# Kernel optimization log

Hardware: AMD Instinct MI355X
Metric: run time of the kernel (lower is better)

Reference implementation:

```python
import jax, jax.numpy as jnp
import numpy as np

N = 50000      # nodes
E = 800000     # edges (before self-loops)
H = 4          # heads
C = 64         # hidden_unit per head
IN = 256       # input_dim
OUT = 64       # output_dim
NEG = 0.2      # LeakyReLU slope in GATConv
EPS = 1e-5     # BatchNorm eps


def setup_inputs() -> dict:
    key = jax.random.key(0)
    ks = jax.random.split(key, 12)
    s = 0.05
    HC = H * C
    return {
        'x': jax.random.normal(ks[0], (N, IN), dtype=jnp.float32),
        'edge_index': jax.random.randint(ks[1], (2, E), 0, N, dtype=jnp.int64),
        # GATConv layer 1
        'W1': jax.random.normal(ks[2], (IN, HC), dtype=jnp.float32) * s,
        'att_src1': jax.random.normal(ks[3], (H, C), dtype=jnp.float32) * s,
        'att_dst1': jax.random.normal(ks[4], (H, C), dtype=jnp.float32) * s,
        'b1': jnp.zeros((HC,), jnp.float32),
        # GATConv layer 2
        'W2': jax.random.normal(ks[5], (HC, HC), dtype=jnp.float32) * s,
        'att_src2': jax.random.normal(ks[6], (H, C), dtype=jnp.float32) * s,
        'att_dst2': jax.random.normal(ks[7], (H, C), dtype=jnp.float32) * s,
        'b2': jnp.zeros((HC,), jnp.float32),
        # BatchNorms
        'g1': jnp.ones((HC,), jnp.float32), 'beta1': jnp.zeros((HC,), jnp.float32),
        'g2': jnp.ones((HC,), jnp.float32), 'beta2': jnp.zeros((HC,), jnp.float32),
        # final Linear
        'Wl': jax.random.normal(ks[8], (HC, OUT), dtype=jnp.float32) * s,
        'bl': jnp.zeros((OUT,), jnp.float32),
    }


def gat_layer(x, src, dst, W, a_src, a_dst, b):
    # x: [N, F_in] -> per-head features [N, H, C]
    xh = (x @ W).reshape(-1, H, C)
    alpha_src = jnp.einsum('nhc,hc->nh', xh, a_src)   # [N, H]
    alpha_dst = jnp.einsum('nhc,hc->nh', xh, a_dst)   # [N, H]
    e = jax.nn.leaky_relu(alpha_src[src] + alpha_dst[dst], NEG)  # [Etot, H]
    # segment softmax over edges grouped by destination node
    m = jax.ops.segment_max(e, dst, num_segments=N)              # [N, H]
    ex = jnp.exp(e - m[dst])
    den = jax.ops.segment_sum(ex, dst, num_segments=N)           # [N, H]
    alpha = ex / (den[dst] + 1e-16)                              # [Etot, H]
    # weighted scatter-add aggregation
    out = jax.ops.segment_sum(alpha[:, :, None] * xh[src], dst, num_segments=N)
    return out.reshape(-1, H * C) + b


def batchnorm(x, g, beta):
    mu = x.mean(axis=0)
    var = x.var(axis=0)
    return (x - mu) * jax.lax.rsqrt(var + EPS) * g + beta


def reference(x, edge_index, W1, att_src1, att_dst1, b1,
              W2, att_src2, att_dst2, b2, g1, beta1, g2, beta2, Wl, bl):
    # GATConv adds self-loops by default
    loops = jnp.arange(N, dtype=edge_index.dtype)
    src = jnp.concatenate([edge_index[0], loops])
    dst = jnp.concatenate([edge_index[1], loops])
    h = batchnorm(gat_layer(x, src, dst, W1, att_src1, att_dst1, b1), g1, beta1)
    # dropout is identity in eval mode
    h = batchnorm(gat_layer(h, src, dst, W2, att_src2, att_dst2, b2), g2, beta2)
    emb = h @ Wl + bl
    out = jax.nn.log_softmax(emb, axis=1)
    return (out, emb)
```

## Files before the change

kernel.cpp:

```cpp
#include <hip/hip_runtime.h>
#include <cstdint>

#define NNODES 50000
#define NEDGES 800000
#define ETOT   (NEDGES + NNODES)
#define HEADS 4
#define CH 64
#define HC 256
#define INDIM 256
#define OUTDIM 64
#define NEG_SLOPE 0.2f
#define BN_EPS 1e-5f
#define NB 128

typedef unsigned short u16;
typedef unsigned int u32;
typedef __attribute__((ext_vector_type(8))) short short8;
typedef __attribute__((ext_vector_type(8))) unsigned short ushort8v;
typedef __attribute__((ext_vector_type(4))) float floatx4;

__device__ inline float bf2f(u16 u) {
    union { unsigned int i; float f; } c;
    c.i = ((unsigned int)u) << 16;
    return c.f;
}
__device__ inline u16 f2bf(float f) {
    union { float f; unsigned int i; } c;
    c.f = f;
    unsigned int u = c.i + 0x7fff + ((c.i >> 16) & 1);
    return (u16)(u >> 16);
}
__device__ __host__ inline int pos256(int b) {
    int h = b >> 6, c = b & 63;
    return h * 64 + (c & 15) * 4 + (c >> 4);
}
__device__ inline void async16(u16* lds, const u16* g) {
    __builtin_amdgcn_global_load_lds(
        (const __attribute__((address_space(1))) unsigned int*)g,
        (__attribute__((address_space(3))) unsigned int*)lds,
        16, 0, 0);
}


__global__ void hist_kernel(const int* __restrict__ ei, int* __restrict__ cnt) {
    int t = blockIdx.x * blockDim.x + threadIdx.x;
    if (t >= ETOT) return;
    int d = (t < NEDGES) ? ei[NEDGES + t] : (t - NEDGES);
    atomicAdd(&cnt[d], 1);
}

__global__ void scan1_kernel(const int* __restrict__ cnt, int* __restrict__ row_off,
                             int* __restrict__ blockSums) {
    __shared__ int tsum[256];
    const int tid = threadIdx.x;
    const int base = blockIdx.x * 4096 + tid * 16;
    int local[16];
    int run = 0;
#pragma unroll
    for (int i = 0; i < 16; ++i) {
        int idx = base + i;
        int v = (idx < NNODES) ? cnt[idx] : 0;
        local[i] = run;
        run += v;
    }
    tsum[tid] = run;
    __syncthreads();
    for (int d = 1; d < 256; d <<= 1) {
        int v = (tid >= d) ? tsum[tid - d] : 0;
        __syncthreads();
        tsum[tid] += v;
        __syncthreads();
    }
    int excl = (tid == 0) ? 0 : tsum[tid - 1];
#pragma unroll
    for (int i = 0; i < 16; ++i) {
        int idx = base + i;
        if (idx < NNODES) row_off[idx] = excl + local[i];
    }
    if (tid == 0) blockSums[blockIdx.x] = tsum[255];
}

__global__ void scan2_kernel(int* __restrict__ row_off, const int* __restrict__ blockSums,
                             int* __restrict__ nxt) {
    __shared__ int sprefix;
    if (threadIdx.x == 0) {
        int p = 0;
        for (int b = 0; b < (int)blockIdx.x; ++b) p += blockSums[b];
        sprefix = p;
    }
    __syncthreads();
    int prefix = sprefix;
    int base = blockIdx.x * 4096 + threadIdx.x * 16;
#pragma unroll
    for (int i = 0; i < 16; ++i) {
        int idx = base + i;
        if (idx < NNODES) {
            int v = row_off[idx] + prefix;
            row_off[idx] = v;
            nxt[idx] = v;
        }
    }
    if (blockIdx.x == 0 && threadIdx.x == 0) row_off[NNODES] = ETOT;
}

#define FILL_S (ETOT / 4)
__global__ void fill_csr_kernel(const int* __restrict__ ei, int* __restrict__ nxt,
                                int* __restrict__ csr_src) {
    int t = blockIdx.x * blockDim.x + threadIdx.x;
    if (t >= FILL_S) return;
    int s[4], d[4], p[4];
#pragma unroll
    for (int k = 0; k < 4; ++k) {
        int e = t + k * FILL_S;
        if (e < NEDGES) { s[k] = ei[e]; d[k] = ei[NEDGES + e]; }
        else            { s[k] = d[k] = e - NEDGES; }
    }
#pragma unroll
    for (int k = 0; k < 4; ++k) p[k] = atomicAdd(&nxt[d[k]], 1);
#pragma unroll
    for (int k = 0; k < 4; ++k) csr_src[p[k]] = s[k];
}


__global__ void wcast_kernel(const float* __restrict__ W, u16* __restrict__ Wt,
                             int K, int Ncols) {
    int t = blockIdx.x * blockDim.x + threadIdx.x;
    if (t >= K * Ncols) return;
    int k = t / Ncols, n = t - k * Ncols;
    Wt[n * K + k] = f2bf(W[t]);
}


template <bool AF32>
__global__ __launch_bounds__(256)
void gemm_gat_kernel(const void* __restrict__ Ap, const u16* __restrict__ Bt,
                     const float* __restrict__ bias,
                     const float* __restrict__ att_s, const float* __restrict__ att_d,
                     u16* __restrict__ xhp, float* __restrict__ asrc,
                     float* __restrict__ adst, int M, int K) {
    __shared__ u16 As[128 * 32];
    __shared__ u16 Bs[128 * 32];
    const int tid = threadIdx.x;
    const int wave = tid >> 6, lane = tid & 63;
    const int q15 = lane & 15, quad = lane >> 4;
    const int rowBase = blockIdx.y * 128;
    const int colBase = blockIdx.x * 128;
    const int waveM = (wave >> 1) * 64, waveN = (wave & 1) * 64;
    const int head = blockIdx.x * 2 + (wave & 1);

    floatx4 acc[4][4];
    floatx4 zero = {0.f, 0.f, 0.f, 0.f};
#pragma unroll
    for (int i = 0; i < 4; ++i)
#pragma unroll
        for (int j = 0; j < 4; ++j) acc[i][j] = zero;

    for (int kt = 0; kt < K; kt += 32) {
        if constexpr (AF32) {
            const float* A32 = (const float*)Ap;
#pragma unroll
            for (int rnd = 0; rnd < 4; ++rnd) {
                int slot = rnd * 256 + tid;
                int r = slot >> 3, c4 = (slot & 7) * 4;
                int ar = rowBase + r; if (ar >= M) ar = M - 1;
                float4 fv = *(const float4*)&A32[(size_t)ar * K + kt + c4];
                ushort4 o;
                o.x = f2bf(fv.x); o.y = f2bf(fv.y); o.z = f2bf(fv.z); o.w = f2bf(fv.w);
                *(ushort4*)&As[r * 32 + c4] = o;
            }
#pragma unroll
            for (int q = 0; q < 2; ++q) {
                int e8 = (wave * 2 + q) * 64 + lane;
                int r = e8 >> 2, c = (e8 & 3) * 8;
                async16(&Bs[(wave * 2 + q) * 512], &Bt[(size_t)(colBase + r) * K + kt + c]);
            }
        } else {
            const u16* A16 = (const u16*)Ap;
#pragma unroll
            for (int q = 0; q < 2; ++q) {
                int e8 = (wave * 2 + q) * 64 + lane;
                int r = e8 >> 2, c = (e8 & 3) * 8;
                int ar = rowBase + r; if (ar >= M) ar = M - 1;
                async16(&As[(wave * 2 + q) * 512], &A16[(size_t)ar * K + kt + c]);
                async16(&Bs[(wave * 2 + q) * 512], &Bt[(size_t)(colBase + r) * K + kt + c]);
            }
        }
        __syncthreads();

        short8 af[4], bfr[4];
#pragma unroll
        for (int i = 0; i < 4; ++i)
            af[i] = *(const short8*)&As[(waveM + i * 16 + q15) * 32 + quad * 8];
#pragma unroll
        for (int j = 0; j < 4; ++j)
            bfr[j] = *(const short8*)&Bs[(waveN + j * 16 + q15) * 32 + quad * 8];
#pragma unroll
        for (int i = 0; i < 4; ++i)
#pragma unroll
            for (int j = 0; j < 4; ++j)
                acc[i][j] = __builtin_amdgcn_mfma_f32_16x16x32_bf16(af[i], bfr[j], acc[i][j], 0, 0, 0);
        __syncthreads();
    }

    float bv[4], atsv[4], atdv[4];
#pragma unroll
    for (int j = 0; j < 4; ++j) {
        int gcol = colBase + waveN + j * 16 + q15;
        bv[j] = bias ? bias[gcol] : 0.f;
        int hc = head * CH + j * 16 + q15;
        atsv[j] = att_s[hc];
        atdv[j] = att_d[hc];
    }
    const int pbase = head * 64 + q15 * 4;

#pragma unroll
    for (int i = 0; i < 4; ++i) {
#pragma unroll
        for (int rr = 0; rr < 4; ++rr) {
            int grow = rowBase + waveM + i * 16 + quad * 4 + rr;
            float v[4];
#pragma unroll
            for (int j = 0; j < 4; ++j) v[j] = acc[i][j][rr] + bv[j];
            float s = v[0] * atsv[0] + v[1] * atsv[1] + v[2] * atsv[2] + v[3] * atsv[3];
            float d = v[0] * atdv[0] + v[1] * atdv[1] + v[2] * atdv[2] + v[3] * atdv[3];
#pragma unroll
            for (int off = 1; off <= 8; off <<= 1) {
                s += __shfl_xor(s, off, 64);
                d += __shfl_xor(d, off, 64);
            }
            ushort4 o;
            o.x = f2bf(v[0]); o.y = f2bf(v[1]); o.z = f2bf(v[2]); o.w = f2bf(v[3]);
            if (grow < M) {
                *(ushort4*)&xhp[(size_t)grow * HC + pbase] = o;
                if (q15 == 0) {
                    asrc[grow * 4 + head] = s;
                    adst[grow * 4 + head] = d;
                }
            }
        }
    }
}


__global__ __launch_bounds__(256)
void aggregate_kernel(const int* __restrict__ row_off, const int* __restrict__ csr_src,
                      const float* __restrict__ asrc, const float* __restrict__ adst,
                      const u16* __restrict__ xhp, const float* __restrict__ bias,
                      u16* __restrict__ out) {
    __shared__ int eb[4][512];
    const int g = threadIdx.x >> 6;
    const int lane = threadIdx.x & 63;
    const int d = blockIdx.x * 4 + g;
    const int eh = lane >> 5;
    const int L = lane & 31;
    const int h = L >> 3;
    const int g8 = L & 7;
    const u32 pb = (u32)(h * 128 + g8 * 16);
    int* my = &eb[g][0];

    const int start = row_off[d], end = row_off[d + 1];
    const float4 ad4 = *(const float4*)&adst[d * 4];
    float acc[8] = {0.f, 0.f, 0.f, 0.f, 0.f, 0.f, 0.f, 0.f};
    float den = 0.f;

#define ACC4(W, Q, J0) { u32 dw_ = (u32)(Q); \
        acc[J0]     += (W) * __int_as_float(dw_ << 16); \
        acc[(J0)+1] += (W) * __int_as_float(dw_ & 0xffff0000u); }

    for (int base = start; base < end; base += 64) {
        const int cnt = min(64, end - base);
        int4 pack = {0, 0, 0, 0};
        int svv = 0;
        if (lane < cnt) {
            svv = csr_src[base + lane];
            float4 as4 = *(const float4*)&asrc[svv * 4];
            float e0 = as4.x + ad4.x; e0 = e0 > 0.f ? e0 : NEG_SLOPE * e0;
            float e1 = as4.y + ad4.y; e1 = e1 > 0.f ? e1 : NEG_SLOPE * e1;
            float e2 = as4.z + ad4.z; e2 = e2 > 0.f ? e2 : NEG_SLOPE * e2;
            float e3 = as4.w + ad4.w; e3 = e3 > 0.f ? e3 : NEG_SLOPE * e3;
            pack.x = __float_as_int(__expf(e0));
            pack.y = __float_as_int(__expf(e1));
            pack.z = __float_as_int(__expf(e2));
            pack.w = __float_as_int(__expf(e3));
        }
        *(int4*)&my[lane * 8] = pack;
        my[lane * 8 + 4] = svv;
        asm volatile("s_waitcnt lgkmcnt(0)" ::: "memory");
        __builtin_amdgcn_sched_barrier(0);

        const int cntp = (cnt + 1) & ~1;
        int k = 0;
        for (; k + 7 < cntp; k += 8) {
            float wv[4]; int sa[4];
#pragma unroll
            for (int p = 0; p < 4; ++p) {
                int idx = (k + 2 * p + eh) * 8;
                wv[p] = __int_as_float(my[idx + h]);
                sa[p] = my[idx + 4];
            }
            int4 gv[4];
#pragma unroll
            for (int p = 0; p < 4; ++p) {
                u32 off = ((u32)sa[p] << 9) + pb;
                gv[p] = *(const int4*)((const char*)xhp + off);
            }
#pragma unroll
            for (int p = 0; p < 4; ++p) {
                float w = wv[p];
                den += w;
                ACC4(w, gv[p].x, 0); ACC4(w, gv[p].y, 2);
                ACC4(w, gv[p].z, 4); ACC4(w, gv[p].w, 6);
            }
        }
        for (; k < cntp; k += 2) {
            int idx = (k + eh) * 8;
            float w = __int_as_float(my[idx + h]);
            int s = my[idx + 4];
            u32 off = ((u32)s << 9) + pb;
            int4 gvv = *(const int4*)((const char*)xhp + off);
            den += w;
            ACC4(w, gvv.x, 0); ACC4(w, gvv.y, 2);
            ACC4(w, gvv.z, 4); ACC4(w, gvv.w, 6);
        }
    }
#undef ACC4

#pragma unroll
    for (int i = 0; i < 8; ++i) acc[i] += __shfl_xor(acc[i], 32, 64);
    den += __shfl_xor(den, 32, 64);

    if (eh == 0) {
        float inv = 1.f / (den + 1e-16f);
        const int cb = h * 64 + g8 * 2;
        ushort8v o;
#pragma unroll
        for (int j = 0; j < 8; ++j)
            o[j] = f2bf(acc[j] * inv + bias[cb + (j >> 2) + (j & 3) * 16]);
        *(ushort8v*)&out[(size_t)d * HC + h * 64 + g8 * 8] = o;
    }
}


__global__ __launch_bounds__(256)
void bn_stats_kernel(const u16* __restrict__ x, float* __restrict__ part) {
    const int tid = threadIdx.x;
    float s[8] = {}, s2[8] = {};
    const size_t total = (size_t)NNODES * HC;
    const size_t stride = (size_t)NB * 256 * 8;
    for (size_t f = ((size_t)blockIdx.x * 256 + tid) * 8; f < total; f += stride) {
        ushort8v v = *(const ushort8v*)&x[f];
#pragma unroll
        for (int i = 0; i < 8; ++i) {
            float t = bf2f(v[i]);
            s[i] += t;
            s2[i] += t * t;
        }
    }
#pragma unroll
    for (int i = 0; i < 8; ++i) {
        s[i] += __shfl_xor(s[i], 32, 64);
        s2[i] += __shfl_xor(s2[i], 32, 64);
    }
    __shared__ float red[4][512];
    const int wave = tid >> 6, lane = tid & 63;
    if (lane < 32) {
#pragma unroll
        for (int i = 0; i < 8; ++i) {
            red[wave][lane * 8 + i] = s[i];
            red[wave][256 + lane * 8 + i] = s2[i];
        }
    }
    __syncthreads();
    for (int j = tid; j < 512; j += 256)
        part[(size_t)blockIdx.x * 512 + j] = red[0][j] + red[1][j] + red[2][j] + red[3][j];
}


__global__ __launch_bounds__(256)
void fold_kernel(const float* __restrict__ W, const float* __restrict__ part,
                 const float* __restrict__ g, const float* __restrict__ beta,
                 const float* __restrict__ baseBias,
                 u16* __restrict__ Wt, float* __restrict__ biasOut, int Ncols) {
    __shared__ float sh[256];
    __shared__ float stat2[2];
    const int b = blockIdx.x;
    const int tid = threadIdx.x;
    if (b < 256) {
        const int p = pos256(b);
        const int wave = tid >> 6, lane = tid & 63;
        if (wave < 2) {
            int off = wave * 256;
            float v = part[(size_t)lane * 512 + off + p] + part[(size_t)(lane + 64) * 512 + off + p];
#pragma unroll
            for (int o = 1; o <= 32; o <<= 1) v += __shfl_xor(v, o, 64);
            if (lane == 0) stat2[wave] = v;
        }
        __syncthreads();
        float mu = stat2[0] * (1.f / NNODES);
        float var = stat2[1] * (1.f / NNODES) - mu * mu;
        float rg = rsqrtf(var + BN_EPS) * g[b];
        for (int n = tid; n < Ncols; n += 256)
            Wt[n * 256 + p] = f2bf(W[b * Ncols + n] * rg);
    } else {
        const int p = pos256(tid);
        float sum = 0.f, sq = 0.f;
        for (int k = 0; k < NB; ++k) {
            sum += part[(size_t)k * 512 + p];
            sq += part[(size_t)k * 512 + 256 + p];
        }
        float mu = sum * (1.f / NNODES);
        float var = sq * (1.f / NNODES) - mu * mu;
        float rg = rsqrtf(var + BN_EPS) * g[tid];
        sh[tid] = beta[tid] - mu * rg;
        __syncthreads();
        if (tid < Ncols) {
            float acc = baseBias ? baseBias[tid] : 0.f;
            for (int k = 0; k < 256; ++k) acc += sh[k] * W[k * Ncols + tid];
            biasOut[tid] = acc;
        }
    }
}


__global__ __launch_bounds__(256)
void final_ls_kernel(const u16* __restrict__ A, const u16* __restrict__ Bt,
                     const float* __restrict__ bias,
                     float* __restrict__ emb, float* __restrict__ out, int M) {
    __shared__ u16 As[128 * 32];
    __shared__ u16 Bs[64 * 32];
    const int tid = threadIdx.x;
    const int wave = tid >> 6, lane = tid & 63;
    const int q15 = lane & 15, quad = lane >> 4;
    const int rowBase = blockIdx.x * 128;

    floatx4 acc[2][4];
    floatx4 zero = {0.f, 0.f, 0.f, 0.f};
#pragma unroll
    for (int i = 0; i < 2; ++i)
#pragma unroll
        for (int j = 0; j < 4; ++j) acc[i][j] = zero;

    for (int kt = 0; kt < 256; kt += 32) {
#pragma unroll
        for (int rnd = 0; rnd < 2; ++rnd) {
            int slot = rnd * 256 + wave * 64 + lane;
            int r = slot >> 2;
            int c = (slot & 3) * 8;
            int ar = rowBase + r; if (ar >= M) ar = M - 1;
            async16(&As[(rnd * 256 + wave * 64) * 8], &A[(size_t)ar * 256 + kt + c]);
        }
        {
            int slot = wave * 64 + lane;
            int r = slot >> 2;
            int c = (slot & 3) * 8;
            async16(&Bs[(wave * 64) * 8], &Bt[(size_t)r * 256 + kt + c]);
        }
        __syncthreads();

        short8 af[2], bfr[4];
#pragma unroll
        for (int i = 0; i < 2; ++i)
            af[i] = *(const short8*)&As[(wave * 32 + i * 16 + q15) * 32 + quad * 8];
#pragma unroll
        for (int j = 0; j < 4; ++j)
            bfr[j] = *(const short8*)&Bs[(j * 16 + q15) * 32 + quad * 8];
#pragma unroll
        for (int i = 0; i < 2; ++i)
#pragma unroll
            for (int j = 0; j < 4; ++j)
                acc[i][j] = __builtin_amdgcn_mfma_f32_16x16x32_bf16(af[i], bfr[j], acc[i][j], 0, 0, 0);
        __syncthreads();
    }

#pragma unroll
    for (int i = 0; i < 2; ++i) {
#pragma unroll
        for (int rr = 0; rr < 4; ++rr) {
            float v[4];
#pragma unroll
            for (int j = 0; j < 4; ++j) v[j] = acc[i][j][rr] + bias[j * 16 + q15];
            float m = fmaxf(fmaxf(v[0], v[1]), fmaxf(v[2], v[3]));
#pragma unroll
            for (int off = 1; off <= 8; off <<= 1) m = fmaxf(m, __shfl_xor(m, off, 64));
            float s = __expf(v[0] - m) + __expf(v[1] - m) + __expf(v[2] - m) + __expf(v[3] - m);
#pragma unroll
            for (int off = 1; off <= 8; off <<= 1) s += __shfl_xor(s, off, 64);
            float ls = m + logf(s);
            int grow = rowBase + wave * 32 + i * 16 + quad * 4 + rr;
            if (grow < M) {
#pragma unroll
                for (int j = 0; j < 4; ++j) {
                    int col = j * 16 + q15;
                    emb[(size_t)grow * OUTDIM + col] = v[j];
                    out[(size_t)grow * OUTDIM + col] = v[j] - ls;
                }
            }
        }
    }
}


extern "C" void kernel_launch(void* const* d_in, const int* in_sizes, int n_in,
                              void* d_out, int out_size, void* d_ws, size_t ws_size,
                              hipStream_t stream) {
    const float* x   = (const float*)d_in[0];
    const int*   ei  = (const int*)d_in[1];
    const float* W1  = (const float*)d_in[2];
    const float* at_s1 = (const float*)d_in[3];
    const float* at_d1 = (const float*)d_in[4];
    const float* b1  = (const float*)d_in[5];
    const float* W2  = (const float*)d_in[6];
    const float* at_s2 = (const float*)d_in[7];
    const float* at_d2 = (const float*)d_in[8];
    const float* b2  = (const float*)d_in[9];
    const float* g1  = (const float*)d_in[10];
    const float* be1 = (const float*)d_in[11];
    const float* g2  = (const float*)d_in[12];
    const float* be2 = (const float*)d_in[13];
    const float* Wl  = (const float*)d_in[14];
    const float* bl  = (const float*)d_in[15];

    float* out = (float*)d_out;
    float* emb = out + (size_t)NNODES * OUTDIM;

    char* ws = (char*)d_ws;
    size_t off = 0;
    auto alloc = [&](size_t bytes) {
        void* p = ws + off;
        off += (bytes + 255) & ~(size_t)255;
        return p;
    };
    int*   cnt     = (int*)alloc((size_t)NNODES * 4);
    int*   row_off = (int*)alloc((size_t)(NNODES + 1) * 4);
    int*   nxt     = (int*)alloc((size_t)NNODES * 4);
    int*   bsums   = (int*)alloc(64 * 4);
    int*   csr_src = (int*)alloc((size_t)ETOT * 4);
    float* asrc    = (float*)alloc((size_t)NNODES * 4 * 4);
    float* adst    = (float*)alloc((size_t)NNODES * 4 * 4);
    u16*   xhp     = (u16*)alloc((size_t)NNODES * HC * 2);
    u16*   ag_bf   = (u16*)alloc((size_t)NNODES * HC * 2);
    u16*   w1t     = (u16*)alloc((size_t)HC * INDIM * 2);
    u16*   w2t     = (u16*)alloc((size_t)HC * HC * 2);
    u16*   wlt     = (u16*)alloc((size_t)OUTDIM * HC * 2);
    float* part    = (float*)alloc((size_t)NB * 512 * 4);
    float* bias2   = (float*)alloc(HC * 4);
    float* blp     = (float*)alloc(OUTDIM * 4);

    const int scanBlocks = (NNODES + 4095) / 4096;
    const int eBlocks = (ETOT + 255) / 256;

    hipMemsetAsync(cnt, 0, (size_t)NNODES * 4, stream);
    hist_kernel<<<eBlocks, 256, 0, stream>>>(ei, cnt);
    scan1_kernel<<<scanBlocks, 256, 0, stream>>>(cnt, row_off, bsums);
    scan2_kernel<<<scanBlocks, 256, 0, stream>>>(row_off, bsums, nxt);
    fill_csr_kernel<<<(FILL_S + 255) / 256, 256, 0, stream>>>(ei, nxt, csr_src);

    wcast_kernel<<<(INDIM * HC + 255) / 256, 256, 0, stream>>>(W1, w1t, INDIM, HC);

    dim3 gemmGrid(2, (NNODES + 127) / 128);

    gemm_gat_kernel<true><<<gemmGrid, 256, 0, stream>>>(x, w1t, nullptr, at_s1, at_d1,
                                                        xhp, asrc, adst, NNODES, INDIM);
    aggregate_kernel<<<NNODES / 4, 256, 0, stream>>>(row_off, csr_src, asrc, adst, xhp, b1, ag_bf);
    bn_stats_kernel<<<NB, 256, 0, stream>>>(ag_bf, part);
    fold_kernel<<<257, 256, 0, stream>>>(W2, part, g1, be1, nullptr, w2t, bias2, HC);

    gemm_gat_kernel<false><<<gemmGrid, 256, 0, stream>>>(ag_bf, w2t, bias2, at_s2, at_d2,
                                                         xhp, asrc, adst, NNODES, HC);
    aggregate_kernel<<<NNODES / 4, 256, 0, stream>>>(row_off, csr_src, asrc, adst, xhp, b2, ag_bf);
    bn_stats_kernel<<<NB, 256, 0, stream>>>(ag_bf, part);
    fold_kernel<<<257, 256, 0, stream>>>(Wl, part, g2, be2, bl, wlt, blp, OUTDIM);

    final_ls_kernel<<<(NNODES + 127) / 128, 256, 0, stream>>>(ag_bf, wlt, blp, emb, out, NNODES);
}
```

Baseline: 495.0 us.

## Merge CSR build and BN stats/fold stages into cooperative grid-synced kernels

Replaces the memset, histogram, two scan kernels, CSR fill and weight cast with one cooperative kernel that separates phases with grid.sync. It also merges each bn_stats and fold pair into one cooperative kernel. The aim is to cut kernel launch overhead and inter-kernel gaps across many small stages. In exchange, the CSR work runs on a fixed grid of 1024 blocks with grid-stride loops, and grid barriers add cost; the scan phases use only a few blocks while the rest wait at the barrier.

```diff
diff --git a/kernel.cpp b/kernel.cpp
--- a/kernel.cpp
+++ b/kernel.cpp
@@ -1,5 +1,8 @@
 #include <hip/hip_runtime.h>
+#include <hip/hip_cooperative_groups.h>
 #include <cstdint>
+
+namespace cg = cooperative_groups;
 
 #define NNODES 50000
 #define NEDGES 800000
@@ -12,6 +15,8 @@
 #define NEG_SLOPE 0.2f
 #define BN_EPS 1e-5f
 #define NB 128
+#define CSR_BLOCKS 1024
+#define CSR_GSZ (CSR_BLOCKS * 256)
 
 typedef unsigned short u16;
 typedef unsigned int u32;
@@ -40,94 +45,109 @@
         (__attribute__((address_space(3))) unsigned int*)lds,
         16, 0, 0);
 }
-
-
-__global__ void hist_kernel(const int* __restrict__ ei, int* __restrict__ cnt) {
-    int t = blockIdx.x * blockDim.x + threadIdx.x;
-    if (t >= ETOT) return;
-    int d = (t < NEDGES) ? ei[NEDGES + t] : (t - NEDGES);
-    atomicAdd(&cnt[d], 1);
-}
-
-__global__ void scan1_kernel(const int* __restrict__ cnt, int* __restrict__ row_off,
-                             int* __restrict__ blockSums) {
+__device__ inline int ld_devi(const int* p) {
+    return __hip_atomic_load(p, __ATOMIC_RELAXED, __HIP_MEMORY_SCOPE_AGENT);
+}
+__device__ inline float ld_devf(const float* p) {
+    return __hip_atomic_load(p, __ATOMIC_RELAXED, __HIP_MEMORY_SCOPE_AGENT);
+}
+
+
+#define FILL_S (ETOT / 4)
+
+__global__ __launch_bounds__(256)
+void csr_build_kernel(const int* __restrict__ ei, int* __restrict__ cnt,
+                      int* __restrict__ row_off, int* __restrict__ nxt,
+                      int* __restrict__ bsums, int* __restrict__ csr_src,
+                      const float* __restrict__ W1, u16* __restrict__ w1t) {
+    cg::grid_group grid = cg::this_grid();
+    const int tid = threadIdx.x;
+    const int gt = blockIdx.x * 256 + tid;
     __shared__ int tsum[256];
-    const int tid = threadIdx.x;
-    const int base = blockIdx.x * 4096 + tid * 16;
-    int local[16];
-    int run = 0;
-#pragma unroll
-    for (int i = 0; i < 16; ++i) {
-        int idx = base + i;
-        int v = (idx < NNODES) ? cnt[idx] : 0;
-        local[i] = run;
-        run += v;
-    }
-    tsum[tid] = run;
-    __syncthreads();
-    for (int d = 1; d < 256; d <<= 1) {
-        int v = (tid >= d) ? tsum[tid - d] : 0;
-        __syncthreads();
-        tsum[tid] += v;
-        __syncthreads();
-    }
-    int excl = (tid == 0) ? 0 : tsum[tid - 1];
-#pragma unroll
-    for (int i = 0; i < 16; ++i) {
-        int idx = base + i;
-        if (idx < NNODES) row_off[idx] = excl + local[i];
-    }
-    if (tid == 0) blockSums[blockIdx.x] = tsum[255];
-}
-
-__global__ void scan2_kernel(int* __restrict__ row_off, const int* __restrict__ blockSums,
-                             int* __restrict__ nxt) {
     __shared__ int sprefix;
-    if (threadIdx.x == 0) {
-        int p = 0;
-        for (int b = 0; b < (int)blockIdx.x; ++b) p += blockSums[b];
-        sprefix = p;
-    }
-    __syncthreads();
-    int prefix = sprefix;
-    int base = blockIdx.x * 4096 + threadIdx.x * 16;
-#pragma unroll
-    for (int i = 0; i < 16; ++i) {
-        int idx = base + i;
-        if (idx < NNODES) {
-            int v = row_off[idx] + prefix;
-            row_off[idx] = v;
-            nxt[idx] = v;
-        }
-    }
-    if (blockIdx.x == 0 && threadIdx.x == 0) row_off[NNODES] = ETOT;
-}
-
-#define FILL_S (ETOT / 4)
-__global__ void fill_csr_kernel(const int* __restrict__ ei, int* __restrict__ nxt,
-                                int* __restrict__ csr_src) {
-    int t = blockIdx.x * blockDim.x + threadIdx.x;
-    if (t >= FILL_S) return;
-    int s[4], d[4], p[4];
-#pragma unroll
-    for (int k = 0; k < 4; ++k) {
-        int e = t + k * FILL_S;
-        if (e < NEDGES) { s[k] = ei[e]; d[k] = ei[NEDGES + e]; }
-        else            { s[k] = d[k] = e - NEDGES; }
-    }
-#pragma unroll
-    for (int k = 0; k < 4; ++k) p[k] = atomicAdd(&nxt[d[k]], 1);
-#pragma unroll
-    for (int k = 0; k < 4; ++k) csr_src[p[k]] = s[k];
-}
-
-
-__global__ void wcast_kernel(const float* __restrict__ W, u16* __restrict__ Wt,
-                             int K, int Ncols) {
-    int t = blockIdx.x * blockDim.x + threadIdx.x;
-    if (t >= K * Ncols) return;
-    int k = t / Ncols, n = t - k * Ncols;
-    Wt[n * K + k] = f2bf(W[t]);
+
+    for (int i = gt; i < NNODES; i += CSR_GSZ) cnt[i] = 0;
+    for (int i = gt; i < INDIM * HC; i += CSR_GSZ) {
+        int k = i >> 8, n = i & 255;
+        w1t[n * INDIM + k] = f2bf(W1[i]);
+    }
+    __threadfence();
+    grid.sync();
+
+    for (int t = gt; t < ETOT; t += CSR_GSZ) {
+        int d = (t < NEDGES) ? ei[NEDGES + t] : (t - NEDGES);
+        atomicAdd(&cnt[d], 1);
+    }
+    __threadfence();
+    grid.sync();
+
+    const int scanBlocks = (NNODES + 4095) / 4096;
+    if ((int)blockIdx.x < scanBlocks) {
+        const int base = blockIdx.x * 4096 + tid * 16;
+        int local[16];
+        int run = 0;
+#pragma unroll
+        for (int i = 0; i < 16; ++i) {
+            int idx = base + i;
+            int v = (idx < NNODES) ? ld_devi(&cnt[idx]) : 0;
+            local[i] = run;
+            run += v;
+        }
+        tsum[tid] = run;
+        __syncthreads();
+        for (int dd = 1; dd < 256; dd <<= 1) {
+            int v = (tid >= dd) ? tsum[tid - dd] : 0;
+            __syncthreads();
+            tsum[tid] += v;
+            __syncthreads();
+        }
+        int excl = (tid == 0) ? 0 : tsum[tid - 1];
+#pragma unroll
+        for (int i = 0; i < 16; ++i) {
+            int idx = base + i;
+            if (idx < NNODES) row_off[idx] = excl + local[i];
+        }
+        if (tid == 0) bsums[blockIdx.x] = tsum[255];
+    }
+    __threadfence();
+    grid.sync();
+
+    if ((int)blockIdx.x < scanBlocks) {
+        if (tid == 0) {
+            int p = 0;
+            for (int b = 0; b < (int)blockIdx.x; ++b) p += ld_devi(&bsums[b]);
+            sprefix = p;
+        }
+        __syncthreads();
+        int prefix = sprefix;
+        int base = blockIdx.x * 4096 + tid * 16;
+#pragma unroll
+        for (int i = 0; i < 16; ++i) {
+            int idx = base + i;
+            if (idx < NNODES) {
+                int v = row_off[idx] + prefix;
+                row_off[idx] = v;
+                nxt[idx] = v;
+            }
+        }
+        if (blockIdx.x == 0 && tid == 0) row_off[NNODES] = ETOT;
+    }
+    __threadfence();
+    grid.sync();
+
+    if (gt < FILL_S) {
+        int s[4], d[4], p[4];
+#pragma unroll
+        for (int k = 0; k < 4; ++k) {
+            int e = gt + k * FILL_S;
+            if (e < NEDGES) { s[k] = ei[e]; d[k] = ei[NEDGES + e]; }
+            else            { s[k] = d[k] = e - NEDGES; }
+        }
+#pragma unroll
+        for (int k = 0; k < 4; ++k) p[k] = atomicAdd(&nxt[d[k]], 1);
+#pragma unroll
+        for (int k = 0; k < 4; ++k) csr_src[p[k]] = s[k];
+    }
 }
 
 
@@ -342,55 +362,57 @@
 
 
 __global__ __launch_bounds__(256)
-void bn_stats_kernel(const u16* __restrict__ x, float* __restrict__ part) {
+void statsfold_kernel(const u16* __restrict__ x, float* __restrict__ part,
+                      const float* __restrict__ W, const float* __restrict__ g,
+                      const float* __restrict__ beta, const float* __restrict__ baseBias,
+                      u16* __restrict__ Wt, float* __restrict__ biasOut, int Ncols) {
+    cg::grid_group grid = cg::this_grid();
     const int tid = threadIdx.x;
-    float s[8] = {}, s2[8] = {};
-    const size_t total = (size_t)NNODES * HC;
-    const size_t stride = (size_t)NB * 256 * 8;
-    for (size_t f = ((size_t)blockIdx.x * 256 + tid) * 8; f < total; f += stride) {
-        ushort8v v = *(const ushort8v*)&x[f];
-#pragma unroll
-        for (int i = 0; i < 8; ++i) {
-            float t = bf2f(v[i]);
-            s[i] += t;
-            s2[i] += t * t;
-        }
-    }
-#pragma unroll
-    for (int i = 0; i < 8; ++i) {
-        s[i] += __shfl_xor(s[i], 32, 64);
-        s2[i] += __shfl_xor(s2[i], 32, 64);
-    }
     __shared__ float red[4][512];
-    const int wave = tid >> 6, lane = tid & 63;
-    if (lane < 32) {
-#pragma unroll
-        for (int i = 0; i < 8; ++i) {
-            red[wave][lane * 8 + i] = s[i];
-            red[wave][256 + lane * 8 + i] = s2[i];
-        }
-    }
-    __syncthreads();
-    for (int j = tid; j < 512; j += 256)
-        part[(size_t)blockIdx.x * 512 + j] = red[0][j] + red[1][j] + red[2][j] + red[3][j];
-}
-
-
-__global__ __launch_bounds__(256)
-void fold_kernel(const float* __restrict__ W, const float* __restrict__ part,
-                 const float* __restrict__ g, const float* __restrict__ beta,
-                 const float* __restrict__ baseBias,
-                 u16* __restrict__ Wt, float* __restrict__ biasOut, int Ncols) {
     __shared__ float sh[256];
     __shared__ float stat2[2];
+
+    if (blockIdx.x < NB) {
+        float s[8] = {}, s2[8] = {};
+        const size_t total = (size_t)NNODES * HC;
+        const size_t stride = (size_t)NB * 256 * 8;
+        for (size_t f = ((size_t)blockIdx.x * 256 + tid) * 8; f < total; f += stride) {
+            ushort8v v = *(const ushort8v*)&x[f];
+#pragma unroll
+            for (int i = 0; i < 8; ++i) {
+                float t = bf2f(v[i]);
+                s[i] += t;
+                s2[i] += t * t;
+            }
+        }
+#pragma unroll
+        for (int i = 0; i < 8; ++i) {
+            s[i] += __shfl_xor(s[i], 32, 64);
+            s2[i] += __shfl_xor(s2[i], 32, 64);
+        }
+        const int wave = tid >> 6, lane = tid & 63;
+        if (lane < 32) {
+#pragma unroll
+            for (int i = 0; i < 8; ++i) {
+                red[wave][lane * 8 + i] = s[i];
+                red[wave][256 + lane * 8 + i] = s2[i];
+            }
+        }
+        __syncthreads();
+        for (int j = tid; j < 512; j += 256)
+            part[(size_t)blockIdx.x * 512 + j] = red[0][j] + red[1][j] + red[2][j] + red[3][j];
+    }
+    __threadfence();
+    grid.sync();
+
     const int b = blockIdx.x;
-    const int tid = threadIdx.x;
     if (b < 256) {
         const int p = pos256(b);
         const int wave = tid >> 6, lane = tid & 63;
         if (wave < 2) {
             int off = wave * 256;
-            float v = part[(size_t)lane * 512 + off + p] + part[(size_t)(lane + 64) * 512 + off + p];
+            float v = ld_devf(&part[(size_t)lane * 512 + off + p]) +
+                      ld_devf(&part[(size_t)(lane + 64) * 512 + off + p]);
 #pragma unroll
             for (int o = 1; o <= 32; o <<= 1) v += __shfl_xor(v, o, 64);
             if (lane == 0) stat2[wave] = v;
@@ -405,8 +427,8 @@
         const int p = pos256(tid);
         float sum = 0.f, sq = 0.f;
         for (int k = 0; k < NB; ++k) {
-            sum += part[(size_t)k * 512 + p];
-            sq += part[(size_t)k * 512 + 256 + p];
+            sum += ld_devf(&part[(size_t)k * 512 + p]);
+            sq += ld_devf(&part[(size_t)k * 512 + 256 + p]);
         }
         float mu = sum * (1.f / NNODES);
         float var = sq * (1.f / NNODES) - mu * mu;
@@ -546,30 +568,36 @@
     float* bias2   = (float*)alloc(HC * 4);
     float* blp     = (float*)alloc(OUTDIM * 4);
 
-    const int scanBlocks = (NNODES + 4095) / 4096;
-    const int eBlocks = (ETOT + 255) / 256;
-
-    hipMemsetAsync(cnt, 0, (size_t)NNODES * 4, stream);
-    hist_kernel<<<eBlocks, 256, 0, stream>>>(ei, cnt);
-    scan1_kernel<<<scanBlocks, 256, 0, stream>>>(cnt, row_off, bsums);
-    scan2_kernel<<<scanBlocks, 256, 0, stream>>>(row_off, bsums, nxt);
-    fill_csr_kernel<<<(FILL_S + 255) / 256, 256, 0, stream>>>(ei, nxt, csr_src);
-
-    wcast_kernel<<<(INDIM * HC + 255) / 256, 256, 0, stream>>>(W1, w1t, INDIM, HC);
+    {
+        void* a[] = {(void*)&ei, (void*)&cnt, (void*)&row_off, (void*)&nxt,
+                     (void*)&bsums, (void*)&csr_src, (void*)&W1, (void*)&w1t};
+        hipLaunchCooperativeKernel((void*)csr_build_kernel, dim3(CSR_BLOCKS), dim3(256),
+                                   a, 0, stream);
+    }
 
     dim3 gemmGrid(2, (NNODES + 127) / 128);
+    const float* nbias = nullptr;
+    int ncols1 = HC, ncols2 = OUTDIM;
 
     gemm_gat_kernel<true><<<gemmGrid, 256, 0, stream>>>(x, w1t, nullptr, at_s1, at_d1,
                                                         xhp, asrc, adst, NNODES, INDIM);
     aggregate_kernel<<<NNODES / 4, 256, 0, stream>>>(row_off, csr_src, asrc, adst, xhp, b1, ag_bf);
-    bn_stats_kernel<<<NB, 256, 0, stream>>>(ag_bf, part);
-    fold_kernel<<<257, 256, 0, stream>>>(W2, part, g1, be1, nullptr, w2t, bias2, HC);
+    {
+        void* a[] = {(void*)&ag_bf, (void*)&part, (void*)&W2, (void*)&g1, (void*)&be1,
+                     (void*)&nbias, (void*)&w2t, (void*)&bias2, (void*)&ncols1};
+        hipLaunchCooperativeKernel((void*)statsfold_kernel, dim3(257), dim3(256),
+                                   a, 0, stream);
+    }
 
     gemm_gat_kernel<false><<<gemmGrid, 256, 0, stream>>>(ag_bf, w2t, bias2, at_s2, at_d2,
                                                          xhp, asrc, adst, NNODES, HC);
     aggregate_kernel<<<NNODES / 4, 256, 0, stream>>>(row_off, csr_src, asrc, adst, xhp, b2, ag_bf);
-    bn_stats_kernel<<<NB, 256, 0, stream>>>(ag_bf, part);
-    fold_kernel<<<257, 256, 0, stream>>>(Wl, part, g2, be2, bl, wlt, blp, OUTDIM);
+    {
+        void* a[] = {(void*)&ag_bf, (void*)&part, (void*)&Wl, (void*)&g2, (void*)&be2,
+                     (void*)&bl, (void*)&wlt, (void*)&blp, (void*)&ncols2};
+        hipLaunchCooperativeKernel((void*)statsfold_kernel, dim3(257), dim3(256),
+                                   a, 0, stream);
+    }
 
     final_ls_kernel<<<(NNODES + 127) / 128, 256, 0, stream>>>(ag_bf, wlt, blp, emb, out, NNODES);
 }
```

After: 1.273 ms. 157% more time.

## Widen GEMM tile to all 256 columns so each A tile loads once

Applied to the files above, without the earlier changes.

The GAT projection GEMM now uses 512-thread blocks with 8 waves covering a 128x256 output tile, so each block computes all four heads for its rows. Before, two column blocks each reloaded and converted the same A rows. This halves A traffic and, for layer 1, halves the fp32-to-bf16 conversion work. In exchange the B tile in LDS doubles, blocks are larger with fewer in flight, and only one block-row grid dimension remains.

```diff
diff --git a/kernel.cpp b/kernel.cpp
--- a/kernel.cpp
+++ b/kernel.cpp
@@ -132,21 +132,21 @@
 
 
 template <bool AF32>
-__global__ __launch_bounds__(256)
+__global__ __launch_bounds__(512)
 void gemm_gat_kernel(const void* __restrict__ Ap, const u16* __restrict__ Bt,
                      const float* __restrict__ bias,
                      const float* __restrict__ att_s, const float* __restrict__ att_d,
                      u16* __restrict__ xhp, float* __restrict__ asrc,
                      float* __restrict__ adst, int M, int K) {
     __shared__ u16 As[128 * 32];
-    __shared__ u16 Bs[128 * 32];
+    __shared__ u16 Bs[256 * 32];
     const int tid = threadIdx.x;
     const int wave = tid >> 6, lane = tid & 63;
     const int q15 = lane & 15, quad = lane >> 4;
-    const int rowBase = blockIdx.y * 128;
-    const int colBase = blockIdx.x * 128;
-    const int waveM = (wave >> 1) * 64, waveN = (wave & 1) * 64;
-    const int head = blockIdx.x * 2 + (wave & 1);
+    const int rowBase = blockIdx.x * 128;
+    const int waveM = (wave >> 2) * 64;
+    const int waveN = (wave & 3) * 64;
+    const int head = wave & 3;
 
     floatx4 acc[4][4];
     floatx4 zero = {0.f, 0.f, 0.f, 0.f};
@@ -158,32 +158,29 @@
     for (int kt = 0; kt < K; kt += 32) {
         if constexpr (AF32) {
             const float* A32 = (const float*)Ap;
-#pragma unroll
-            for (int rnd = 0; rnd < 4; ++rnd) {
-                int slot = rnd * 256 + tid;
-                int r = slot >> 3, c4 = (slot & 7) * 4;
+            {
+                int r = tid >> 2, c = (tid & 3) * 8;
                 int ar = rowBase + r; if (ar >= M) ar = M - 1;
-                float4 fv = *(const float4*)&A32[(size_t)ar * K + kt + c4];
-                ushort4 o;
-                o.x = f2bf(fv.x); o.y = f2bf(fv.y); o.z = f2bf(fv.z); o.w = f2bf(fv.w);
-                *(ushort4*)&As[r * 32 + c4] = o;
-            }
-#pragma unroll
-            for (int q = 0; q < 2; ++q) {
-                int e8 = (wave * 2 + q) * 64 + lane;
-                int r = e8 >> 2, c = (e8 & 3) * 8;
-                async16(&Bs[(wave * 2 + q) * 512], &Bt[(size_t)(colBase + r) * K + kt + c]);
+                const float* src = &A32[(size_t)ar * K + kt + c];
+                float4 f0 = *(const float4*)src;
+                float4 f1 = *(const float4*)(src + 4);
+                ushort8v o;
+                o[0] = f2bf(f0.x); o[1] = f2bf(f0.y); o[2] = f2bf(f0.z); o[3] = f2bf(f0.w);
+                o[4] = f2bf(f1.x); o[5] = f2bf(f1.y); o[6] = f2bf(f1.z); o[7] = f2bf(f1.w);
+                *(ushort8v*)&As[r * 32 + c] = o;
             }
         } else {
             const u16* A16 = (const u16*)Ap;
-#pragma unroll
-            for (int q = 0; q < 2; ++q) {
-                int e8 = (wave * 2 + q) * 64 + lane;
-                int r = e8 >> 2, c = (e8 & 3) * 8;
-                int ar = rowBase + r; if (ar >= M) ar = M - 1;
-                async16(&As[(wave * 2 + q) * 512], &A16[(size_t)ar * K + kt + c]);
-                async16(&Bs[(wave * 2 + q) * 512], &Bt[(size_t)(colBase + r) * K + kt + c]);
-            }
+            int e8 = tid;
+            int r = e8 >> 2, c = (e8 & 3) * 8;
+            int ar = rowBase + r; if (ar >= M) ar = M - 1;
+            async16(&As[(wave * 64) * 8], &A16[(size_t)ar * K + kt + c]);
+        }
+#pragma unroll
+        for (int q = 0; q < 2; ++q) {
+            int e8 = q * 512 + wave * 64 + lane;
+            int r = e8 >> 2, c = (e8 & 3) * 8;
+            async16(&Bs[(q * 512 + wave * 64) * 8], &Bt[(size_t)r * K + kt + c]);
         }
         __syncthreads();
 
@@ -205,11 +202,10 @@
     float bv[4], atsv[4], atdv[4];
 #pragma unroll
     for (int j = 0; j < 4; ++j) {
-        int gcol = colBase + waveN + j * 16 + q15;
+        int gcol = waveN + j * 16 + q15;
         bv[j] = bias ? bias[gcol] : 0.f;
-        int hc = head * CH + j * 16 + q15;
-        atsv[j] = att_s[hc];
-        atdv[j] = att_d[hc];
+        atsv[j] = att_s[gcol];
+        atdv[j] = att_d[gcol];
     }
     const int pbase = head * 64 + q15 * 4;
 
@@ -557,16 +553,16 @@
 
     wcast_kernel<<<(INDIM * HC + 255) / 256, 256, 0, stream>>>(W1, w1t, INDIM, HC);
 
-    dim3 gemmGrid(2, (NNODES + 127) / 128);
-
-    gemm_gat_kernel<true><<<gemmGrid, 256, 0, stream>>>(x, w1t, nullptr, at_s1, at_d1,
-                                                        xhp, asrc, adst, NNODES, INDIM);
+    const int gemmBlocks = (NNODES + 127) / 128;
+
+    gemm_gat_kernel<true><<<gemmBlocks, 512, 0, stream>>>(x, w1t, nullptr, at_s1, at_d1,
+                                                          xhp, asrc, adst, NNODES, INDIM);
     aggregate_kernel<<<NNODES / 4, 256, 0, stream>>>(row_off, csr_src, asrc, adst, xhp, b1, ag_bf);
     bn_stats_kernel<<<NB, 256, 0, stream>>>(ag_bf, part);
     fold_kernel<<<257, 256, 0, stream>>>(W2, part, g1, be1, nullptr, w2t, bias2, HC);
 
-    gemm_gat_kernel<false><<<gemmGrid, 256, 0, stream>>>(ag_bf, w2t, bias2, at_s2, at_d2,
-                                                         xhp, asrc, adst, NNODES, HC);
+    gemm_gat_kernel<false><<<gemmBlocks, 512, 0, stream>>>(ag_bf, w2t, bias2, at_s2, at_d2,
+                                                           xhp, asrc, adst, NNODES, HC);
     aggregate_kernel<<<NNODES / 4, 256, 0, stream>>>(row_off, csr_src, asrc, adst, xhp, b2, ag_bf);
     bn_stats_kernel<<<NB, 256, 0, stream>>>(ag_bf, part);
     fold_kernel<<<257, 256, 0, stream>>>(Wl, part, g2, be2, bl, wlt, blp, OUTDIM);
```

Result: faster. 483.4 us (-2.3%).
